# Kernel tuning notes

Measured on AMD Instinct MI355X. Metric: run time of the kernel, lower is better.

## Reference

```python
import jax, jax.numpy as jnp
import numpy as np
import math

B, S, D_MODEL, H = 4, 256, 2048, 256
HEAD_DIM = D_MODEL // H  # 8


def setup_inputs() -> dict:
    key = jax.random.key(0)
    ks = jax.random.split(key, 10)
    w_scale = 0.02
    inp = {
        "x": jax.random.normal(ks[0], (B, S, D_MODEL), dtype=jnp.float32),
        "phase_shift": jax.random.normal(ks[1], (H, 1, 1), dtype=jnp.float32),
        "Wq": jax.random.normal(ks[2], (D_MODEL, D_MODEL), dtype=jnp.float32) * w_scale,
        "bq": jnp.zeros((D_MODEL,), dtype=jnp.float32),
        "Wk": jax.random.normal(ks[3], (D_MODEL, D_MODEL), dtype=jnp.float32) * w_scale,
        "bk": jnp.zeros((D_MODEL,), dtype=jnp.float32),
        "Wv": jax.random.normal(ks[4], (D_MODEL, D_MODEL), dtype=jnp.float32) * w_scale,
        "bv": jnp.zeros((D_MODEL,), dtype=jnp.float32),
        "Wo": jax.random.normal(ks[5], (D_MODEL, D_MODEL), dtype=jnp.float32) * w_scale,
        "bo": jnp.zeros((D_MODEL,), dtype=jnp.float32),
    }
    return inp


def _forward(x, phase_shift, Wq, bq, Wk, bk, Wv, bv, Wo, bo):
    b, s, dm = x.shape
    h = phase_shift.shape[0]
    d = dm // h
    # projections (torch Linear with random weights; stored as [in,out])
    q = (x @ Wq + bq).reshape(b, s, h, d)
    k = (x @ Wk + bk).reshape(b, s, h, d)
    v = (x @ Wv + bv).reshape(b, s, h, d)
    # complex phase rotation: q *= exp(+i phi), k *= exp(-i phi)
    # phase_shift (h,1,1) broadcasts against (b,s,h,d) -> varies along the s dim (requires s==h)
    c = jnp.cos(phase_shift)  # (h,1,1)
    sn = jnp.sin(phase_shift)
    qr, qi = q * c, q * sn          # Re/Im of rotated q
    kr, ki = k * c, -(k * sn)       # Re/Im of rotated k
    scale = 1.0 / math.sqrt(d)
    # per-(b,s) head-mixing scores: [b,s,h,h], complex matmul split into real/imag
    sr = (jnp.einsum('bshd,bsgd->bshg', qr, kr)
          - jnp.einsum('bshd,bsgd->bshg', qi, ki)) * scale
    si = (jnp.einsum('bshd,bsgd->bshg', qr, ki)
          + jnp.einsum('bshd,bsgd->bshg', qi, kr)) * scale  # analytically 0 (phases cancel)
    attn_r = jax.nn.softmax(sr, axis=-1)
    attn_i = jax.nn.softmax(si, axis=-1)  # faithful dual softmax; v is real so only
    # Re(attention @ v) = attn_r @ v reaches the output (.real is taken before o_proj)
    del attn_i
    out = jnp.einsum('bshg,bsgd->bshd', attn_r, v).reshape(b, s, dm)
    return out @ Wo + bo


def reference(x, phase_shift, Wq, bq, Wk, bk, Wv, bv, Wo, bo):
    return _forward(x, phase_shift, Wq, bq, Wk, bk, Wv, bv, Wo, bo)
```

## Files before the change

### kernel.cpp

```cpp
#include <hip/hip_runtime.h>
#include <math.h>

#define M_TOK 1024
#define DM    2048
#define NH    256
#define HD    8
#define SCALE 0.35355339059327373f

typedef _Float16 f16x8 __attribute__((ext_vector_type(8)));
typedef _Float16 f16x4 __attribute__((ext_vector_type(4)));
typedef float    f32x4 __attribute__((ext_vector_type(4)));

__global__ __launch_bounds__(256) void cast_x(
    const float* __restrict__ in, _Float16* __restrict__ out, int n8)
{
    int i = blockIdx.x * blockDim.x + threadIdx.x;
    if (i >= n8) return;
    const float4 a = ((const float4*)in)[2 * i];
    const float4 b = ((const float4*)in)[2 * i + 1];
    f16x8 v;
    v[0] = (_Float16)a.x; v[1] = (_Float16)a.y; v[2] = (_Float16)a.z; v[3] = (_Float16)a.w;
    v[4] = (_Float16)b.x; v[5] = (_Float16)b.y; v[6] = (_Float16)b.z; v[7] = (_Float16)b.w;
    ((f16x8*)out)[i] = v;
}

__global__ __launch_bounds__(256) void castT(
    const float* __restrict__ W0, const float* __restrict__ W1,
    const float* __restrict__ W2, const float* __restrict__ W3,
    _Float16* __restrict__ T0, _Float16* __restrict__ T1,
    _Float16* __restrict__ T2, _Float16* __restrict__ T3)
{
    __shared__ float t[64][65];
    const int z = blockIdx.z;
    const float* W = (z == 0) ? W0 : (z == 1) ? W1 : (z == 2) ? W2 : W3;
    _Float16*    T = (z == 0) ? T0 : (z == 1) ? T1 : (z == 2) ? T2 : T3;

    const int nb = blockIdx.x * 64;
    const int kb = blockIdx.y * 64;
    const int tid = threadIdx.x;
    const int tr  = tid >> 4;
    const int tc  = (tid & 15) << 2;

    #pragma unroll
    for (int rr = 0; rr < 4; ++rr) {
        const int k = kb + rr * 16 + tr;
        const float4 v = *(const float4*)&W[(size_t)k * DM + nb + tc];
        t[rr * 16 + tr][tc + 0] = v.x;
        t[rr * 16 + tr][tc + 1] = v.y;
        t[rr * 16 + tr][tc + 2] = v.z;
        t[rr * 16 + tr][tc + 3] = v.w;
    }
    __syncthreads();
    #pragma unroll
    for (int rr = 0; rr < 4; ++rr) {
        const int n = nb + rr * 16 + tr;
        f16x4 v;
        #pragma unroll
        for (int j = 0; j < 4; ++j)
            v[j] = (_Float16)t[tc + j][rr * 16 + tr];
        *(f16x4*)&T[(size_t)n * DM + kb + tc] = v;
    }
}

template<int TI, bool F16OUT>
__global__ __launch_bounds__(256) void gemm_t(
    const _Float16* __restrict__ A,
    const _Float16* __restrict__ Bt0, const float* __restrict__ b0, void* __restrict__ C0,
    const _Float16* __restrict__ Bt1, const float* __restrict__ b1, void* __restrict__ C1,
    const _Float16* __restrict__ Bt2, const float* __restrict__ b2, void* __restrict__ C2)
{
    constexpr int BM = 32 * TI;
    constexpr int NA = 2 * TI;
    constexpr int NB = 8;
    constexpr int PC = (NA + NB) / 4;

    __shared__ _Float16 As[BM * 32];
    __shared__ _Float16 Bs[128 * 32];

    const int which = blockIdx.x >> 4;
    const int bn    = (blockIdx.x & 15) * 128;
    const int bm    = blockIdx.y * BM;

    const _Float16* Bt   = (which == 0) ? Bt0 : (which == 1) ? Bt1 : Bt2;
    const float*    bias = (which == 0) ? b0  : (which == 1) ? b1  : b2;
    void*           C    = (which == 0) ? C0  : (which == 1) ? C1  : C2;

    const int tid  = threadIdx.x;
    const int lane = tid & 63;
    const int wv   = tid >> 6;
    const int wr   = (wv >> 1) * 16 * TI;
    const int wc   = (wv & 1) * 64;
    const int lr   = lane & 15;
    const int lk   = lane >> 4;

    const _Float16* gsrc[PC];
    _Float16*       ldst[PC];
    #pragma unroll
    for (int p = 0; p < PC; ++p) {
        const int c = wv * PC + p;
        if (c < NA) {
            ldst[p] = &As[c * 512];
            gsrc[p] = A + (size_t)(bm + c * 16 + (lane >> 2)) * DM + (lane & 3) * 8;
        } else {
            ldst[p] = &Bs[(c - NA) * 512];
            gsrc[p] = Bt + (size_t)(bn + (c - NA) * 16 + (lane >> 2)) * DM + (lane & 3) * 8;
        }
    }

    f32x4 acc[TI][4] = {};

    for (int k0 = 0; k0 < DM; k0 += 32) {
        __syncthreads();
        #pragma unroll
        for (int p = 0; p < PC; ++p) {
            __builtin_amdgcn_global_load_lds(
                (const __attribute__((address_space(1))) void*)gsrc[p],
                (__attribute__((address_space(3))) void*)ldst[p], 16, 0, 0);
            gsrc[p] += 32;
        }
        __syncthreads();

        f16x8 aF[TI], bF[4];
        #pragma unroll
        for (int i = 0; i < TI; ++i)
            aF[i] = *(const f16x8*)&As[(wr + i * 16 + lr) * 32 + lk * 8];
        #pragma unroll
        for (int j = 0; j < 4; ++j)
            bF[j] = *(const f16x8*)&Bs[(wc + j * 16 + lr) * 32 + lk * 8];

        #pragma unroll
        for (int i = 0; i < TI; ++i)
            #pragma unroll
            for (int j = 0; j < 4; ++j)
                acc[i][j] = __builtin_amdgcn_mfma_f32_16x16x32_f16(aF[i], bF[j], acc[i][j], 0, 0, 0);
    }

    #pragma unroll
    for (int i = 0; i < TI; ++i) {
        #pragma unroll
        for (int j = 0; j < 4; ++j) {
            const int col = bn + wc + j * 16 + lr;
            const float bv = bias[col];
            #pragma unroll
            for (int r = 0; r < 4; ++r) {
                const int row = bm + wr + i * 16 + lk * 4 + r;
                const float v = acc[i][j][r] + bv;
                if (F16OUT)
                    ((_Float16*)C)[(size_t)row * DM + col] = (_Float16)v;
                else
                    ((float*)C)[(size_t)row * DM + col] = v;
            }
        }
    }
}

__global__ __launch_bounds__(256) void attn_mfma(
    const _Float16* __restrict__ Qh, const _Float16* __restrict__ Kh,
    const _Float16* __restrict__ Vh, _Float16* __restrict__ Oh)
{
    __shared__ _Float16 Vt[8][264];
    __shared__ _Float16 Al[256][72];
    __shared__ _Float16 Ot[256][8];

    const int t    = blockIdx.x;
    const int tid  = threadIdx.x;
    const int lane = tid & 63;
    const int wv   = tid >> 6;
    const int col  = lane & 15;
    const int quad = lane >> 4;
    const int hbase = wv * 64;

    const _Float16* qb = Qh + (size_t)t * DM;
    const _Float16* kb = Kh + (size_t)t * DM;
    const _Float16* vb = Vh + (size_t)t * DM;

    {
        const f16x8 v = *(const f16x8*)(vb + tid * 8);
        #pragma unroll
        for (int d = 0; d < 8; ++d) Vt[d][tid] = v[d];
    }

    f16x8 qf[4];
    #pragma unroll
    for (int ht = 0; ht < 4; ++ht) {
        f16x8 v = {};
        if (quad == 0)
            v = *(const f16x8*)(qb + (hbase + ht * 16 + col) * 8);
        #pragma unroll
        for (int j = 0; j < 8; ++j) qf[ht][j] = v[j] * (_Float16)SCALE;
    }

    __syncthreads();

    const f32x4 zf = {};
    float rsum[4] = {};
    f32x4 oacc[4] = {};

    #pragma unroll 1
    for (int c = 0; c < 4; ++c) {
        const int gchunk = c * 64;

        f16x8 kf[4];
        #pragma unroll
        for (int gt = 0; gt < 4; ++gt) {
            f16x8 v = {};
            if (quad == 0)
                v = *(const f16x8*)(kb + (gchunk + gt * 16 + col) * 8);
            kf[gt] = v;
        }

        f32x4 s[4][4];
        #pragma unroll
        for (int gt = 0; gt < 4; ++gt)
            #pragma unroll
            for (int ht = 0; ht < 4; ++ht)
                s[gt][ht] = __builtin_amdgcn_mfma_f32_16x16x32_f16(kf[gt], qf[ht], zf, 0, 0, 0);

        #pragma unroll
        for (int gt = 0; gt < 4; ++gt) {
            #pragma unroll
            for (int ht = 0; ht < 4; ++ht) {
                f16x4 e4;
                #pragma unroll
                for (int r = 0; r < 4; ++r) {
                    e4[r] = (_Float16)__expf(s[gt][ht][r]);
                    rsum[ht] += (float)e4[r];
                }
                *(f16x4*)&Al[hbase + ht * 16 + col][gt * 16 + quad * 4] = e4;
            }
        }

        #pragma unroll
        for (int ks = 0; ks < 2; ++ks) {
            f16x8 vf = {};
            if (col < 8)
                vf = *(const f16x8*)&Vt[col][gchunk + ks * 32 + quad * 8];
            #pragma unroll
            for (int ht = 0; ht < 4; ++ht) {
                const f16x8 af = *(const f16x8*)&Al[hbase + ht * 16 + col][ks * 32 + quad * 8];
                oacc[ht] = __builtin_amdgcn_mfma_f32_16x16x32_f16(af, vf, oacc[ht], 0, 0, 0);
            }
        }
    }

    #pragma unroll
    for (int ht = 0; ht < 4; ++ht) {
        rsum[ht] += __shfl_xor(rsum[ht], 16, 64);
        rsum[ht] += __shfl_xor(rsum[ht], 32, 64);
    }

    #pragma unroll
    for (int ht = 0; ht < 4; ++ht) {
        #pragma unroll
        for (int r = 0; r < 4; ++r) {
            const float sh = __shfl(rsum[ht], quad * 4 + r, 64);
            const float v  = oacc[ht][r] / sh;
            if (col < 8)
                Ot[hbase + ht * 16 + quad * 4 + r][col] = (_Float16)v;
        }
    }
    const f16x8 ov = *(const f16x8*)&Ot[tid][0];
    *(f16x8*)(Oh + (size_t)t * DM + tid * 8) = ov;
}

extern "C" void kernel_launch(void* const* d_in, const int* in_sizes, int n_in,
                              void* d_out, int out_size, void* d_ws, size_t ws_size,
                              hipStream_t stream)
{
    const float* x  = (const float*)d_in[0];
    const float* Wq = (const float*)d_in[2];
    const float* bq = (const float*)d_in[3];
    const float* Wk = (const float*)d_in[4];
    const float* bk = (const float*)d_in[5];
    const float* Wv = (const float*)d_in[6];
    const float* bv = (const float*)d_in[7];
    const float* Wo = (const float*)d_in[8];
    const float* bo = (const float*)d_in[9];
    float* out = (float*)d_out;

    char* ws = (char*)d_ws;
    _Float16* xh  = (_Float16*)(ws);
    _Float16* Wtq = (_Float16*)(ws + (4u  << 20));
    _Float16* Wtk = (_Float16*)(ws + (12u << 20));
    _Float16* Wtv = (_Float16*)(ws + (20u << 20));
    _Float16* Wto = (_Float16*)(ws + (28u << 20));
    _Float16* Qh  = (_Float16*)(ws + (36u << 20));
    _Float16* Kh  = (_Float16*)(ws + (40u << 20));
    _Float16* Vh  = (_Float16*)(ws + (44u << 20));
    _Float16* Oh  = (_Float16*)(ws + (48u << 20));

    const dim3 blk(256);

    cast_x<<<dim3((M_TOK * DM / 8 + 255) / 256), blk, 0, stream>>>(x, xh, M_TOK * DM / 8);

    castT<<<dim3(32, 32, 4), blk, 0, stream>>>(Wq, Wk, Wv, Wo, Wtq, Wtk, Wtv, Wto);

    gemm_t<4, true><<<dim3(48, 8), blk, 0, stream>>>(xh,
        Wtq, bq, (void*)Qh,
        Wtk, bk, (void*)Kh,
        Wtv, bv, (void*)Vh);

    attn_mfma<<<dim3(M_TOK), blk, 0, stream>>>(Qh, Kh, Vh, Oh);

    gemm_t<2, false><<<dim3(16, 16), blk, 0, stream>>>(Oh,
        Wto, bo, (void*)out,
        Wto, bo, (void*)out,
        Wto, bo, (void*)out);
}
```

Before: 222.6 us.

## Merge cast kernels into one launch and use 8-wave GEMM blocks

Folds the x fp16 cast into the weight transpose-cast kernel as an extra grid z-slice, which removes one kernel launch. The GEMM now runs 512 threads (8 waves) per block, with each wave owning 32 output columns instead of 64. Global-to-LDS load chunks are redistributed across the 8 waves, with a validity guard for the unused slots. This raises per-block wave parallelism and latency hiding but halves per-wave reuse of the A fragments, and it issues more LDS reads per MFMA.

```diff
diff --git a/kernel.cpp b/kernel.cpp
--- a/kernel.cpp
+++ b/kernel.cpp
@@ -11,35 +11,35 @@
 typedef _Float16 f16x4 __attribute__((ext_vector_type(4)));
 typedef float    f32x4 __attribute__((ext_vector_type(4)));
 
-__global__ __launch_bounds__(256) void cast_x(
-    const float* __restrict__ in, _Float16* __restrict__ out, int n8)
-{
-    int i = blockIdx.x * blockDim.x + threadIdx.x;
-    if (i >= n8) return;
-    const float4 a = ((const float4*)in)[2 * i];
-    const float4 b = ((const float4*)in)[2 * i + 1];
-    f16x8 v;
-    v[0] = (_Float16)a.x; v[1] = (_Float16)a.y; v[2] = (_Float16)a.z; v[3] = (_Float16)a.w;
-    v[4] = (_Float16)b.x; v[5] = (_Float16)b.y; v[6] = (_Float16)b.z; v[7] = (_Float16)b.w;
-    ((f16x8*)out)[i] = v;
-}
-
-__global__ __launch_bounds__(256) void castT(
+__global__ __launch_bounds__(256) void prep(
+    const float* __restrict__ x, _Float16* __restrict__ xh,
     const float* __restrict__ W0, const float* __restrict__ W1,
     const float* __restrict__ W2, const float* __restrict__ W3,
     _Float16* __restrict__ T0, _Float16* __restrict__ T1,
     _Float16* __restrict__ T2, _Float16* __restrict__ T3)
 {
     __shared__ float t[64][65];
-    const int z = blockIdx.z;
+    const int tid = threadIdx.x;
+    const int z   = blockIdx.z;
+
+    if (z == 4) {
+        const int i = (blockIdx.y * 32 + blockIdx.x) * 256 + tid;
+        const float4 a = ((const float4*)x)[2 * i];
+        const float4 b = ((const float4*)x)[2 * i + 1];
+        f16x8 v;
+        v[0] = (_Float16)a.x; v[1] = (_Float16)a.y; v[2] = (_Float16)a.z; v[3] = (_Float16)a.w;
+        v[4] = (_Float16)b.x; v[5] = (_Float16)b.y; v[6] = (_Float16)b.z; v[7] = (_Float16)b.w;
+        ((f16x8*)xh)[i] = v;
+        return;
+    }
+
     const float* W = (z == 0) ? W0 : (z == 1) ? W1 : (z == 2) ? W2 : W3;
     _Float16*    T = (z == 0) ? T0 : (z == 1) ? T1 : (z == 2) ? T2 : T3;
 
     const int nb = blockIdx.x * 64;
     const int kb = blockIdx.y * 64;
-    const int tid = threadIdx.x;
-    const int tr  = tid >> 4;
-    const int tc  = (tid & 15) << 2;
+    const int tr = tid >> 4;
+    const int tc = (tid & 15) << 2;
 
     #pragma unroll
     for (int rr = 0; rr < 4; ++rr) {
@@ -63,7 +63,7 @@
 }
 
 template<int TI, bool F16OUT>
-__global__ __launch_bounds__(256) void gemm_t(
+__global__ __launch_bounds__(512) void gemm_t(
     const _Float16* __restrict__ A,
     const _Float16* __restrict__ Bt0, const float* __restrict__ b0, void* __restrict__ C0,
     const _Float16* __restrict__ Bt1, const float* __restrict__ b1, void* __restrict__ C1,
@@ -72,7 +72,8 @@
     constexpr int BM = 32 * TI;
     constexpr int NA = 2 * TI;
     constexpr int NB = 8;
-    constexpr int PC = (NA + NB) / 4;
+    constexpr int NC = NA + NB;
+    constexpr int PC = (NC + 7) / 8;
 
     __shared__ _Float16 As[BM * 32];
     __shared__ _Float16 Bs[128 * 32];
@@ -88,57 +89,63 @@
     const int tid  = threadIdx.x;
     const int lane = tid & 63;
     const int wv   = tid >> 6;
-    const int wr   = (wv >> 1) * 16 * TI;
-    const int wc   = (wv & 1) * 64;
+    const int wr   = (wv >> 2) * (16 * TI);
+    const int wc   = (wv & 3) * 32;
     const int lr   = lane & 15;
     const int lk   = lane >> 4;
 
+    bool            vld[PC];
     const _Float16* gsrc[PC];
     _Float16*       ldst[PC];
     #pragma unroll
     for (int p = 0; p < PC; ++p) {
-        const int c = wv * PC + p;
+        const int c = p * 8 + wv;
+        vld[p] = (c < NC);
         if (c < NA) {
             ldst[p] = &As[c * 512];
             gsrc[p] = A + (size_t)(bm + c * 16 + (lane >> 2)) * DM + (lane & 3) * 8;
-        } else {
+        } else if (c < NC) {
             ldst[p] = &Bs[(c - NA) * 512];
             gsrc[p] = Bt + (size_t)(bn + (c - NA) * 16 + (lane >> 2)) * DM + (lane & 3) * 8;
-        }
-    }
-
-    f32x4 acc[TI][4] = {};
+        } else {
+            ldst[p] = &As[0];
+            gsrc[p] = A;
+        }
+    }
+
+    f32x4 acc[TI][2] = {};
 
     for (int k0 = 0; k0 < DM; k0 += 32) {
         __syncthreads();
         #pragma unroll
         for (int p = 0; p < PC; ++p) {
-            __builtin_amdgcn_global_load_lds(
-                (const __attribute__((address_space(1))) void*)gsrc[p],
-                (__attribute__((address_space(3))) void*)ldst[p], 16, 0, 0);
+            if (vld[p])
+                __builtin_amdgcn_global_load_lds(
+                    (const __attribute__((address_space(1))) void*)gsrc[p],
+                    (__attribute__((address_space(3))) void*)ldst[p], 16, 0, 0);
             gsrc[p] += 32;
         }
         __syncthreads();
 
-        f16x8 aF[TI], bF[4];
+        f16x8 aF[TI], bF[2];
         #pragma unroll
         for (int i = 0; i < TI; ++i)
             aF[i] = *(const f16x8*)&As[(wr + i * 16 + lr) * 32 + lk * 8];
         #pragma unroll
-        for (int j = 0; j < 4; ++j)
+        for (int j = 0; j < 2; ++j)
             bF[j] = *(const f16x8*)&Bs[(wc + j * 16 + lr) * 32 + lk * 8];
 
         #pragma unroll
         for (int i = 0; i < TI; ++i)
             #pragma unroll
-            for (int j = 0; j < 4; ++j)
+            for (int j = 0; j < 2; ++j)
                 acc[i][j] = __builtin_amdgcn_mfma_f32_16x16x32_f16(aF[i], bF[j], acc[i][j], 0, 0, 0);
     }
 
     #pragma unroll
     for (int i = 0; i < TI; ++i) {
         #pragma unroll
-        for (int j = 0; j < 4; ++j) {
+        for (int j = 0; j < 2; ++j) {
             const int col = bn + wc + j * 16 + lr;
             const float bv = bias[col];
             #pragma unroll
@@ -289,20 +296,17 @@
     _Float16* Vh  = (_Float16*)(ws + (44u << 20));
     _Float16* Oh  = (_Float16*)(ws + (48u << 20));
 
-    const dim3 blk(256);
-
-    cast_x<<<dim3((M_TOK * DM / 8 + 255) / 256), blk, 0, stream>>>(x, xh, M_TOK * DM / 8);
-
-    castT<<<dim3(32, 32, 4), blk, 0, stream>>>(Wq, Wk, Wv, Wo, Wtq, Wtk, Wtv, Wto);
-
-    gemm_t<4, true><<<dim3(48, 8), blk, 0, stream>>>(xh,
+    prep<<<dim3(32, 32, 5), dim3(256), 0, stream>>>(
+        x, xh, Wq, Wk, Wv, Wo, Wtq, Wtk, Wtv, Wto);
+
+    gemm_t<4, true><<<dim3(48, 8), dim3(512), 0, stream>>>(xh,
         Wtq, bq, (void*)Qh,
         Wtk, bk, (void*)Kh,
         Wtv, bv, (void*)Vh);
 
-    attn_mfma<<<dim3(M_TOK), blk, 0, stream>>>(Qh, Kh, Vh, Oh);
-
-    gemm_t<2, false><<<dim3(16, 16), blk, 0, stream>>>(Oh,
+    attn_mfma<<<dim3(M_TOK), dim3(256), 0, stream>>>(Qh, Kh, Vh, Oh);
+
+    gemm_t<2, false><<<dim3(16, 16), dim3(512), 0, stream>>>(Oh,
         Wto, bo, (void*)out,
         Wto, bo, (void*)out,
         Wto, bo, (void*)out);
```

Result: no change. 222.1 us (-0.2%).
